# Performance work log

Measured on AMD Instinct MI355X. Metric: run time of the kernel, lower is better.

Reference implementation:

```python
import jax, jax.numpy as jnp
import numpy as np

DRUG_NUM, DIS_NUM, HIDE_DIM = 60000, 40000, 128
HOPS, N_LAYERS, N_HEADS, FFN_DIM, N_EDGES = 7, 2, 4, 512, 800000
N_NODES = DRUG_NUM + DIS_NUM


def _ln(x, s, b, eps=1e-5):
    m = jnp.mean(x, axis=-1, keepdims=True)
    v = jnp.var(x, axis=-1, keepdims=True)
    return (x - m) * jax.lax.rsqrt(v + eps) * s + b


def setup_inputs() -> dict:
    ks = jax.random.split(jax.random.key(0), 16)
    L, D, F = N_LAYERS, HIDE_DIM, FFN_DIM
    sd = 0.05  # param init scale
    n = lambda k, shape, s=sd: jax.random.normal(k, shape, jnp.float32) * s
    kk = jax.random.split(ks[15], 12)
    return {
        'ifTraining': 0,
        'uid': jax.random.randint(ks[0], (256,), 0, DRUG_NUM, jnp.int64 if jax.config.jax_enable_x64 else jnp.int32),
        'iid': jax.random.randint(ks[1], (256,), 0, DIS_NUM, jnp.int64 if jax.config.jax_enable_x64 else jnp.int32),
        'norm': 1,
        'drug_emb': n(ks[2], (DRUG_NUM, D), 0.1),
        'dis_emb': n(ks[3], (DIS_NUM, D), 0.1),
        'edge_src': jax.random.randint(ks[4], (N_EDGES,), 0, N_NODES, jnp.int32),
        'edge_dst': jax.random.randint(ks[5], (N_EDGES,), 0, N_NODES, jnp.int32),
        'edge_val': jax.random.uniform(ks[6], (N_EDGES,), jnp.float32) * 0.1,  # normalized adj values
        'att_w': n(ks[7], (D, D)), 'att_b': jnp.zeros((D,), jnp.float32),
        'ln1_s': jnp.ones((L, D), jnp.float32), 'ln1_b': jnp.zeros((L, D), jnp.float32),
        'q_w': n(kk[0], (L, D, D)), 'q_b': jnp.zeros((L, D), jnp.float32),
        'k_w': n(kk[1], (L, D, D)), 'k_b': jnp.zeros((L, D), jnp.float32),
        'v_w': n(kk[2], (L, D, D)), 'v_b': jnp.zeros((L, D), jnp.float32),
        'o_w': n(kk[3], (L, D, D)), 'o_b': jnp.zeros((L, D), jnp.float32),
        'ln2_s': jnp.ones((L, D), jnp.float32), 'ln2_b': jnp.zeros((L, D), jnp.float32),
        'f1_w': n(kk[4], (L, D, F)), 'f1_b': jnp.zeros((L, F), jnp.float32),
        'f2_w': n(kk[5], (L, F, D)), 'f2_b': jnp.zeros((L, D), jnp.float32),
        'fln_s': jnp.ones((D,), jnp.float32), 'fln_b': jnp.zeros((D,), jnp.float32),
        'attn_w': n(kk[6], (2 * D, 1)), 'attn_b': jnp.zeros((1,), jnp.float32),
    }


def reference(ifTraining, uid, iid, norm, drug_emb, dis_emb, edge_src, edge_dst, edge_val,
              att_w, att_b, ln1_s, ln1_b, q_w, q_b, k_w, k_b, v_w, v_b, o_w, o_b,
              ln2_s, ln2_b, f1_w, f1_b, f2_w, f2_b, fln_s, fln_b, attn_w, attn_b):
    N, D, S, dh = N_NODES, HIDE_DIM, HOPS + 1, HIDE_DIM // N_HEADS
    # ---- re_features: K sparse-adjacency hops over concatenated embeddings ----
    x = jnp.concatenate([drug_emb, dis_emb], axis=0)  # [N, D]
    feats = [x]
    for _ in range(HOPS):
        msgs = x[edge_src] * edge_val[:, None]          # [E, D] gather
        x = jax.ops.segment_sum(msgs, edge_dst, num_segments=N)  # [N, D] scatter-add
        feats.append(x)
    nf = jnp.stack(feats, axis=1)                        # [N, S, D]
    # ---- graph-transformer over the hop sequence (eval: dropout = identity) ----
    h = nf @ att_w + att_b                               # [N, S, D]
    for l in range(N_LAYERS):
        y = _ln(h, ln1_s[l], ln1_b[l])
        q = (y @ q_w[l] + q_b[l]).reshape(N, S, N_HEADS, dh)
        k = (y @ k_w[l] + k_b[l]).reshape(N, S, N_HEADS, dh)
        v = (y @ v_w[l] + v_b[l]).reshape(N, S, N_HEADS, dh)
        a = jnp.einsum('nshd,nthd->nhst', q, k) * (dh ** -0.5)
        a = jax.nn.softmax(a, axis=-1)                   # [N, H, S, S]
        y = jnp.einsum('nhst,nthd->nshd', a, v).reshape(N, S, D)
        h = h + (y @ o_w[l] + o_b[l])
        y = _ln(h, ln2_s[l], ln2_b[l])
        h = h + (jax.nn.gelu(y @ f1_w[l] + f1_b[l]) @ f2_w[l] + f2_b[l])
    out = _ln(h, fln_s, fln_b)
    # ---- readout: node token + softmax attention over hop tokens ----
    node = out[:, 0, :]                                  # [N, D]
    neigh = out[:, 1:, :]                                # [N, HOPS, D]
    target = jnp.broadcast_to(node[:, None, :], neigh.shape)
    att = jnp.concatenate([target, neigh], axis=-1) @ attn_w + attn_b  # [N, HOPS, 1]
    att = jax.nn.softmax(att, axis=1)
    final = node + jnp.sum(neigh * att, axis=1)          # [N, D]
    return final[:DRUG_NUM], final[DRUG_NUM:]
```

## Files before the change

kernel.cpp:

```cpp
#include <hip/hip_runtime.h>
#include <hip/hip_bf16.h>

typedef __hip_bfloat16 bf16;
typedef __attribute__((ext_vector_type(8))) short s16x8;
typedef __attribute__((ext_vector_type(4))) float f32x4;

#define NDRUG 60000
#define NDIS  40000
#define NN    100000
#define DIM   128
#define NHOPS 7
#define NEDGE 800000
#define NSB   98

__device__ __forceinline__ float u2f(unsigned short u) {
    union { unsigned int i; float f; } c; c.i = ((unsigned int)u) << 16; return c.f;
}
__device__ __forceinline__ ushort f2u(float f) {
    bf16 h = __float2bfloat16(f);
    return *reinterpret_cast<ushort*>(&h);
}


__global__ void k_init(const float* __restrict__ drug, const float* __restrict__ dis,
                       ushort* __restrict__ nf) {
    int i = blockIdx.x * 256 + threadIdx.x;
    if (i >= NN * 32) return;
    int n = i >> 5, g = (i & 31) << 2;
    const float* sp = (n < NDRUG) ? drug + (size_t)n * 128 + g
                                  : dis + (size_t)(n - NDRUG) * 128 + g;
    float4 v = *(const float4*)sp;
    ushort4 o;
    o.x = f2u(v.x); o.y = f2u(v.y); o.z = f2u(v.z); o.w = f2u(v.w);
    *(ushort4*)(nf + (size_t)n * 1024 + g) = o;
}

__global__ void k_count(const int* __restrict__ edst, int* __restrict__ cnt) {
    int e = blockIdx.x * 256 + threadIdx.x;
    if (e < NEDGE) atomicAdd(&cnt[edst[e]], 1);
}

__global__ void k_scanA(const int* __restrict__ cnt, int* __restrict__ incl,
                        int* __restrict__ btot) {
    __shared__ int part[1024];
    int b = blockIdx.x, t = threadIdx.x;
    int i = b * 1024 + t;
    part[t] = (i < NN) ? cnt[i] : 0;
    __syncthreads();
    for (int o = 1; o < 1024; o <<= 1) {
        int u = (t >= o) ? part[t - o] : 0;
        __syncthreads();
        part[t] += u;
        __syncthreads();
    }
    if (i < NN) incl[i] = part[t];
    if (t == 1023) btot[b] = part[1023];
}

__global__ void k_scanB(const int* __restrict__ btot, int* __restrict__ boff) {
    if (threadIdx.x == 0) {
        int run = 0;
        for (int b = 0; b < NSB; b++) { boff[b] = run; run += btot[b]; }
        boff[NSB] = run;
    }
}

__global__ void k_scanC(const int* __restrict__ cnt, const int* __restrict__ incl,
                        const int* __restrict__ boff, int* __restrict__ rp) {
    int i = blockIdx.x * 256 + threadIdx.x;
    if (i < NN) rp[i] = incl[i] - cnt[i] + boff[i >> 10];
    if (i == 0) rp[NN] = boff[NSB];
}

__global__ void k_copyrp(const int* __restrict__ rp, int* __restrict__ cur) {
    int i = blockIdx.x * 256 + threadIdx.x;
    if (i < NN) cur[i] = rp[i];
}

__global__ void k_scatter(const int* __restrict__ esrc, const int* __restrict__ edst,
                          const float* __restrict__ eval, int* __restrict__ cur,
                          int* __restrict__ ssrc, float* __restrict__ sval) {
    int e = blockIdx.x * 256 + threadIdx.x;
    if (e >= NEDGE) return;
    int d = edst[e];
    int pos = atomicAdd(&cur[d], 1);
    ssrc[pos] = esrc[e];
    sval[pos] = eval[e];
}

__global__ void k_hopg(ushort* __restrict__ nf, const int* __restrict__ rp,
                       const int* __restrict__ ssrc, const float* __restrict__ sval, int s) {
    int t = blockIdx.x * 256 + threadIdx.x;
    if (t >= NN * 32) return;
    int n = t >> 5, d0 = (t & 31) << 2;
    int e0 = rp[n], e1 = rp[n + 1];
    float4 a = make_float4(0.f, 0.f, 0.f, 0.f);
    for (int e = e0; e < e1; e++) {
        int src = ssrc[e];
        float val = sval[e];
        ushort4 u = *(const ushort4*)(nf + (size_t)src * 1024 + (size_t)(s - 1) * 128 + d0);
        a.x += u2f(u.x) * val; a.y += u2f(u.y) * val;
        a.z += u2f(u.z) * val; a.w += u2f(u.w) * val;
    }
    ushort4 o;
    o.x = f2u(a.x); o.y = f2u(a.y); o.z = f2u(a.z); o.w = f2u(a.w);
    *(ushort4*)(nf + (size_t)n * 1024 + (size_t)s * 128 + d0) = o;
}


__global__ void k_pack(const float* __restrict__ W, ushort* __restrict__ P, int K, int Nout) {
    int idx = blockIdx.x * 256 + threadIdx.x;
    int tot = (Nout >> 4) * (K >> 3) * 16;
    if (idx >= tot) return;
    int c = idx & 15;
    int r = idx >> 4;
    int kb = r % (K >> 3);
    int nt = r / (K >> 3);
    ushort o[8];
    #pragma unroll
    for (int i = 0; i < 8; i++)
        o[i] = f2u(W[(size_t)(kb * 8 + i) * Nout + nt * 16 + c]);
    uint4 v;
    v.x = (uint)o[0] | ((uint)o[1] << 16);
    v.y = (uint)o[2] | ((uint)o[3] << 16);
    v.z = (uint)o[4] | ((uint)o[5] << 16);
    v.w = (uint)o[6] | ((uint)o[7] << 16);
    *(uint4*)(P + (size_t)idx * 8) = v;
}

__global__ void k_catb(const float* __restrict__ qb, const float* __restrict__ kb,
                       const float* __restrict__ vb, float* __restrict__ o) {
    int i = threadIdx.x;
    o[i] = (i < 128) ? qb[i] : ((i < 256) ? kb[i - 128] : vb[i - 256]);
}


template <int ACT, int ADD, int OUTBF, int NTPW>
__global__ void k_mgemm(const ushort* __restrict__ X, const ushort* __restrict__ Wp,
                        const float* __restrict__ bias, void* __restrict__ Yv,
                        int M, int K, int Nout) {
    int w = threadIdx.x >> 6, lane = threadIdx.x & 63;
    int lr = lane & 15, lg = lane >> 4;
    int m0 = blockIdx.x * 16;
    int kb8 = K >> 3;
    int row = m0 + lr; if (row > M - 1) row = M - 1;
    const ushort* ap = X + (size_t)row * K + lg * 8;
    f32x4 acc[NTPW] = {};
    for (int k0 = 0; k0 < K; k0 += 32, ap += 32) {
        s16x8 af = *(const s16x8*)ap;
        int kb = (k0 >> 3) + lg;
        #pragma unroll
        for (int t = 0; t < NTPW; t++) {
            int nt = w + t * 4;
            const ushort* bp = Wp + (((size_t)nt * kb8 + kb) * 16 + lr) * 8;
            s16x8 bf_ = *(const s16x8*)bp;
            acc[t] = __builtin_amdgcn_mfma_f32_16x16x32_bf16(af, bf_, acc[t], 0, 0, 0);
        }
    }
    #pragma unroll
    for (int t = 0; t < NTPW; t++) {
        int n = (w + t * 4) * 16 + lr;
        float bv = bias[n];
        #pragma unroll
        for (int j = 0; j < 4; j++) {
            int m = m0 + lg * 4 + j;
            if (m >= M) continue;
            float v = acc[t][j] + bv;
            if (ACT == 1) {
                float x = v;
                float z = 0.7978845608028654f * (x + 0.044715f * x * x * x);
                v = x / (1.0f + __expf(-2.0f * z));
            }
            if (OUTBF) {
                ((ushort*)Yv)[(size_t)m * Nout + n] = f2u(v);
            } else if (ADD) {
                ((float*)Yv)[(size_t)m * Nout + n] += v;
            } else {
                ((float*)Yv)[(size_t)m * Nout + n] = v;
            }
        }
    }
}


__global__ void k_layer(float* __restrict__ H,
                        const ushort* __restrict__ Wqkv, const ushort* __restrict__ Wo,
                        const ushort* __restrict__ Wf1, const ushort* __restrict__ Wf2,
                        const float* __restrict__ s1v, const float* __restrict__ b1v,
                        const float* __restrict__ bqkv, const float* __restrict__ bo,
                        const float* __restrict__ s2v, const float* __restrict__ b2v,
                        const float* __restrict__ bf1, const float* __restrict__ bf2,
                        int M) {
    __shared__ float  h[16][132];
    __shared__ ushort ylds[16][136];
    __shared__ ushort big[16][520];
    __shared__ float  as_[2][256];
    int tid = threadIdx.x;
    int w = tid >> 6, lane = tid & 63;
    int lr = lane & 15, lg = lane >> 4;
    int m0 = blockIdx.x * 16;

    #pragma unroll
    for (int i = 0; i < 2; i++) {
        int gi = i * 256 + tid;
        int row = gi >> 5, c4 = (gi & 31) << 2;
        int grow = m0 + row; if (grow > M - 1) grow = M - 1;
        *(float4*)&h[row][c4] = *(const float4*)(H + (size_t)grow * 128 + c4);
    }
    __syncthreads();

    #pragma unroll
    for (int i = 0; i < 4; i++) {
        int row = w * 4 + i;
        float2 x = *(const float2*)&h[row][lane * 2];
        float sum = x.x + x.y, sq = x.x * x.x + x.y * x.y;
        #pragma unroll
        for (int o = 32; o; o >>= 1) { sum += __shfl_xor(sum, o); sq += __shfl_xor(sq, o); }
        float mean = sum * (1.f / 128.f);
        float inv = rsqrtf(sq * (1.f / 128.f) - mean * mean + 1e-5f);
        float y0 = (x.x - mean) * inv * s1v[lane * 2 + 0] + b1v[lane * 2 + 0];
        float y1 = (x.y - mean) * inv * s1v[lane * 2 + 1] + b1v[lane * 2 + 1];
        *(uint*)&ylds[row][lane * 2] = (uint)f2u(y0) | ((uint)f2u(y1) << 16);
    }
    __syncthreads();

    {
        f32x4 acc[6] = {};
        for (int k0 = 0; k0 < 128; k0 += 32) {
            s16x8 af = *(const s16x8*)&ylds[lr][lg * 8 + k0];
            int kb = (k0 >> 3) + lg;
            #pragma unroll
            for (int t = 0; t < 6; t++) {
                int nt = w + t * 4;
                const ushort* bp = Wqkv + (((size_t)nt * 16 + kb) * 16 + lr) * 8;
                s16x8 bf_ = *(const s16x8*)bp;
                acc[t] = __builtin_amdgcn_mfma_f32_16x16x32_bf16(af, bf_, acc[t], 0, 0, 0);
            }
        }
        #pragma unroll
        for (int t = 0; t < 6; t++) {
            int n = (w + t * 4) * 16 + lr;
            float bv = bqkv[n];
            #pragma unroll
            for (int j = 0; j < 4; j++) big[lg * 4 + j][n] = f2u(acc[t][j] + bv);
        }
    }
    __syncthreads();

    if (w < 2) {
        int hh = lane >> 4, s_ = (lane >> 1) & 7, p = lane & 1;
        const float scale = 0.17677669529663687f;
        float dots[4];
        float mx = -1e30f;
        #pragma unroll
        for (int t4 = 0; t4 < 4; t4++) {
            int t = p * 4 + t4;
            float dot = 0.f;
            #pragma unroll
            for (int d = 0; d < 32; d++)
                dot += u2f(big[w * 8 + s_][hh * 32 + d]) * u2f(big[w * 8 + t][128 + hh * 32 + d]);
            dots[t4] = dot * scale;
            mx = fmaxf(mx, dots[t4]);
        }
        mx = fmaxf(mx, __shfl_xor(mx, 1));
        float sum = 0.f, e4[4];
        #pragma unroll
        for (int t4 = 0; t4 < 4; t4++) { e4[t4] = __expf(dots[t4] - mx); sum += e4[t4]; }
        sum += __shfl_xor(sum, 1);
        float rinv = 1.f / sum;
        #pragma unroll
        for (int t4 = 0; t4 < 4; t4++) as_[w][hh * 64 + s_ * 8 + p * 4 + t4] = e4[t4] * rinv;
    }
    __syncthreads();

    {
        int nd = w & 1, hf = w >> 1;
        #pragma unroll
        for (int i = 0; i < 8; i++) {
            int o = hf * 512 + i * 64 + lane;
            int ss = o >> 7, rem = o & 127, h2 = rem >> 5, dd = rem & 31;
            float accv = 0.f;
            #pragma unroll
            for (int t = 0; t < 8; t++)
                accv += as_[nd][h2 * 64 + ss * 8 + t] * u2f(big[nd * 8 + t][256 + h2 * 32 + dd]);
            ylds[nd * 8 + ss][rem] = f2u(accv);
        }
    }
    __syncthreads();

    {
        f32x4 acc[2] = {};
        for (int k0 = 0; k0 < 128; k0 += 32) {
            s16x8 af = *(const s16x8*)&ylds[lr][lg * 8 + k0];
            int kb = (k0 >> 3) + lg;
            #pragma unroll
            for (int t = 0; t < 2; t++) {
                int nt = w + t * 4;
                const ushort* bp = Wo + (((size_t)nt * 16 + kb) * 16 + lr) * 8;
                s16x8 bf_ = *(const s16x8*)bp;
                acc[t] = __builtin_amdgcn_mfma_f32_16x16x32_bf16(af, bf_, acc[t], 0, 0, 0);
            }
        }
        #pragma unroll
        for (int t = 0; t < 2; t++) {
            int n = (w + t * 4) * 16 + lr;
            float bv = bo[n];
            #pragma unroll
            for (int j = 0; j < 4; j++) h[lg * 4 + j][n] += acc[t][j] + bv;
        }
    }
    __syncthreads();

    #pragma unroll
    for (int i = 0; i < 4; i++) {
        int row = w * 4 + i;
        float2 x = *(const float2*)&h[row][lane * 2];
        float sum = x.x + x.y, sq = x.x * x.x + x.y * x.y;
        #pragma unroll
        for (int o = 32; o; o >>= 1) { sum += __shfl_xor(sum, o); sq += __shfl_xor(sq, o); }
        float mean = sum * (1.f / 128.f);
        float inv = rsqrtf(sq * (1.f / 128.f) - mean * mean + 1e-5f);
        float y0 = (x.x - mean) * inv * s2v[lane * 2 + 0] + b2v[lane * 2 + 0];
        float y1 = (x.y - mean) * inv * s2v[lane * 2 + 1] + b2v[lane * 2 + 1];
        *(uint*)&ylds[row][lane * 2] = (uint)f2u(y0) | ((uint)f2u(y1) << 16);
    }
    __syncthreads();

    {
        f32x4 acc[8] = {};
        for (int k0 = 0; k0 < 128; k0 += 32) {
            s16x8 af = *(const s16x8*)&ylds[lr][lg * 8 + k0];
            int kb = (k0 >> 3) + lg;
            #pragma unroll
            for (int t = 0; t < 8; t++) {
                int nt = w + t * 4;
                const ushort* bp = Wf1 + (((size_t)nt * 16 + kb) * 16 + lr) * 8;
                s16x8 bf_ = *(const s16x8*)bp;
                acc[t] = __builtin_amdgcn_mfma_f32_16x16x32_bf16(af, bf_, acc[t], 0, 0, 0);
            }
        }
        #pragma unroll
        for (int t = 0; t < 8; t++) {
            int n = (w + t * 4) * 16 + lr;
            float bv = bf1[n];
            #pragma unroll
            for (int j = 0; j < 4; j++) {
                float x = acc[t][j] + bv;
                float z = 0.7978845608028654f * (x + 0.044715f * x * x * x);
                big[lg * 4 + j][n] = f2u(x / (1.0f + __expf(-2.0f * z)));
            }
        }
    }
    __syncthreads();

    {
        f32x4 acc[2] = {};
        for (int k0 = 0; k0 < 512; k0 += 32) {
            s16x8 af = *(const s16x8*)&big[lr][lg * 8 + k0];
            int kb = (k0 >> 3) + lg;
            #pragma unroll
            for (int t = 0; t < 2; t++) {
                int nt = w + t * 4;
                const ushort* bp = Wf2 + (((size_t)nt * 64 + kb) * 16 + lr) * 8;
                s16x8 bf_ = *(const s16x8*)bp;
                acc[t] = __builtin_amdgcn_mfma_f32_16x16x32_bf16(af, bf_, acc[t], 0, 0, 0);
            }
        }
        #pragma unroll
        for (int t = 0; t < 2; t++) {
            int n = (w + t * 4) * 16 + lr;
            float bv = bf2[n];
            #pragma unroll
            for (int j = 0; j < 4; j++) h[lg * 4 + j][n] += acc[t][j] + bv;
        }
    }
    __syncthreads();

    #pragma unroll
    for (int i = 0; i < 2; i++) {
        int gi = i * 256 + tid;
        int row = gi >> 5, c4 = (gi & 31) << 2;
        int grow = m0 + row;
        if (grow < M) *(float4*)(H + (size_t)grow * 128 + c4) = *(const float4*)&h[row][c4];
    }
}


__global__ void k_pool(const float* __restrict__ Hc, const float* __restrict__ fs,
                       const float* __restrict__ fb, const float* __restrict__ aw,
                       const float* __restrict__ ab, float* __restrict__ out,
                       int Nc, int n0g) {
    int w = threadIdx.x >> 6, lane = threadIdx.x & 63;
    int nl = blockIdx.x * 4 + w;
    if (nl >= Nc) return;
    const float* hp = Hc + (size_t)nl * 1024;
    float s0 = fs[lane * 2], s1 = fs[lane * 2 + 1];
    float b0 = fb[lane * 2], b1 = fb[lane * 2 + 1];
    float2 yl[8];
    #pragma unroll
    for (int s = 0; s < 8; s++) {
        float2 x = *(const float2*)(hp + s * DIM + lane * 2);
        float sum = x.x + x.y, sq = x.x * x.x + x.y * x.y;
        #pragma unroll
        for (int o = 32; o; o >>= 1) { sum += __shfl_xor(sum, o); sq += __shfl_xor(sq, o); }
        float mean = sum * (1.f / 128.f);
        float inv = rsqrtf(sq * (1.f / 128.f) - mean * mean + 1e-5f);
        yl[s].x = (x.x - mean) * inv * s0 + b0;
        yl[s].y = (x.y - mean) * inv * s1 + b1;
    }
    float awn0 = aw[lane * 2], awn1 = aw[lane * 2 + 1];
    float awh0 = aw[128 + lane * 2], awh1 = aw[128 + lane * 2 + 1];
    float abv = ab[0];
    float lg[7];
    #pragma unroll
    for (int s = 0; s < 7; s++) {
        float part = yl[0].x * awn0 + yl[0].y * awn1 + yl[s + 1].x * awh0 + yl[s + 1].y * awh1;
        #pragma unroll
        for (int o = 32; o; o >>= 1) part += __shfl_xor(part, o);
        lg[s] = part + abv;
    }
    float mx = lg[0];
    #pragma unroll
    for (int s = 1; s < 7; s++) mx = fmaxf(mx, lg[s]);
    float sum = 0.f;
    #pragma unroll
    for (int s = 0; s < 7; s++) { lg[s] = __expf(lg[s] - mx); sum += lg[s]; }
    float rinv = 1.f / sum;
    float2 f = yl[0];
    #pragma unroll
    for (int s = 0; s < 7; s++) { f.x += lg[s] * rinv * yl[s + 1].x; f.y += lg[s] * rinv * yl[s + 1].y; }
    size_t ob = (size_t)(n0g + nl) * DIM + lane * 2;
    out[ob + 0] = f.x;
    out[ob + 1] = f.y;
}


extern "C" void kernel_launch(void* const* d_in, const int* in_sizes, int n_in,
                              void* d_out, int out_size, void* d_ws, size_t ws_size,
                              hipStream_t stream) {
    const float* drug  = (const float*)d_in[4];
    const float* dis   = (const float*)d_in[5];
    const int*   esrc  = (const int*)d_in[6];
    const int*   edst  = (const int*)d_in[7];
    const float* eval  = (const float*)d_in[8];
    const float* att_w = (const float*)d_in[9];
    const float* att_b = (const float*)d_in[10];
    const float* ln1_s = (const float*)d_in[11];
    const float* ln1_b = (const float*)d_in[12];
    const float* q_w   = (const float*)d_in[13];
    const float* q_b   = (const float*)d_in[14];
    const float* k_w   = (const float*)d_in[15];
    const float* k_b   = (const float*)d_in[16];
    const float* v_w   = (const float*)d_in[17];
    const float* v_b   = (const float*)d_in[18];
    const float* o_w   = (const float*)d_in[19];
    const float* o_b   = (const float*)d_in[20];
    const float* ln2_s = (const float*)d_in[21];
    const float* ln2_b = (const float*)d_in[22];
    const float* f1_w  = (const float*)d_in[23];
    const float* f1_b  = (const float*)d_in[24];
    const float* f2_w  = (const float*)d_in[25];
    const float* f2_b  = (const float*)d_in[26];
    const float* fln_s = (const float*)d_in[27];
    const float* fln_b = (const float*)d_in[28];
    const float* aw    = (const float*)d_in[29];
    const float* ab    = (const float*)d_in[30];
    float* out = (float*)d_out;

    char* ws = (char*)d_ws;
    size_t nfB = (size_t)NN * 1024 * 2;
    ushort* nf = (ushort*)ws;
    size_t off = (nfB + 255) & ~(size_t)255;

    ushort* wpk = (ushort*)(ws + off);
    size_t offCsr = off + (1 << 20);
    int*   rp   = (int*)(ws + offCsr);
    int*   cnt  = rp + (NN + 1);
    int*   ssrc = cnt + NN;
    float* sval = (float*)(ssrc + NEDGE);
    int*   incl = (int*)(sval + NEDGE);
    int*   btot = incl + NN;
    int*   boff = btot + 128;
    size_t csrInts = (size_t)(NN + 1) + NN + NEDGE + NEDGE + NN + 256;
    size_t off2 = offCsr + ((csrInts * 4 + 255) & ~(size_t)255);

    size_t scratchB = (ws_size > off2) ? ws_size - off2 : 0;
    long long ncMax = (long long)(scratchB / 4096);
    ncMax &= ~1LL;
    if (ncMax < 2) ncMax = 2;
    int Nc = (int)((ncMax < NN) ? ncMax : NN);
    int nchunks = (NN + Nc - 1) / Nc;
    Nc = (NN + nchunks - 1) / nchunks;
    if (Nc & 1) Nc++;
    float* hbuf = (float*)(ws + off2);

    size_t wpAtt = 0;
    size_t wpQKV[2], wpO[2], wpF1[2], wpF2[2];
    {
        size_t p = 16384;
        for (int l = 0; l < 2; l++) {
            wpQKV[l] = p; p += 49152;
            wpO[l]   = p; p += 16384;
            wpF1[l]  = p; p += 65536;
            wpF2[l]  = p; p += 65536;
        }
    }
    float* qkvB = (float*)(wpk + 409600);

    {
        int b128 = (16384 / 8 + 255) / 256;
        int b512 = (65536 / 8 + 255) / 256;
        k_pack<<<b128, 256, 0, stream>>>(att_w, wpk + wpAtt, 128, 128);
        for (int l = 0; l < 2; l++) {
            k_pack<<<b128, 256, 0, stream>>>(q_w + (size_t)l * 16384, wpk + wpQKV[l], 128, 128);
            k_pack<<<b128, 256, 0, stream>>>(k_w + (size_t)l * 16384, wpk + wpQKV[l] + 16384, 128, 128);
            k_pack<<<b128, 256, 0, stream>>>(v_w + (size_t)l * 16384, wpk + wpQKV[l] + 32768, 128, 128);
            k_pack<<<b128, 256, 0, stream>>>(o_w + (size_t)l * 16384, wpk + wpO[l], 128, 128);
            k_pack<<<b512, 256, 0, stream>>>(f1_w + (size_t)l * 65536, wpk + wpF1[l], 128, 512);
            k_pack<<<b512, 256, 0, stream>>>(f2_w + (size_t)l * 65536, wpk + wpF2[l], 512, 128);
            k_catb<<<1, 384, 0, stream>>>(q_b + l * 128, k_b + l * 128, v_b + l * 128, qkvB + l * 384);
        }
    }

    (void)hipMemsetAsync(cnt, 0, (size_t)NN * 4, stream);
    k_count<<<(NEDGE + 255) / 256, 256, 0, stream>>>(edst, cnt);
    k_scanA<<<NSB, 1024, 0, stream>>>(cnt, incl, btot);
    k_scanB<<<1, 64, 0, stream>>>(btot, boff);
    k_scanC<<<(NN + 255) / 256, 256, 0, stream>>>(cnt, incl, boff, rp);
    k_copyrp<<<(NN + 255) / 256, 256, 0, stream>>>(rp, cnt);
    k_scatter<<<(NEDGE + 255) / 256, 256, 0, stream>>>(esrc, edst, eval, cnt, ssrc, sval);

    k_init<<<(NN * 32 + 255) / 256, 256, 0, stream>>>(drug, dis, nf);
    for (int s = 1; s <= NHOPS; s++)
        k_hopg<<<(NN * 32 + 255) / 256, 256, 0, stream>>>(nf, rp, ssrc, sval, s);

    for (int c = 0; c < nchunks; c++) {
        int cn0 = c * Nc;
        int cn = NN - cn0; if (cn > Nc) cn = Nc;
        if (cn <= 0) break;
        int Mc = cn * 8;
        int mb = (Mc + 15) / 16;
        int nb = (cn + 3) / 4;

        k_mgemm<0, 0, 0, 2><<<mb, 256, 0, stream>>>(nf + (size_t)cn0 * 1024, wpk + wpAtt,
                                                    att_b, hbuf, Mc, 128, 128);
        for (int l = 0; l < 2; l++) {
            k_layer<<<mb, 256, 0, stream>>>(hbuf, wpk + wpQKV[l], wpk + wpO[l],
                                            wpk + wpF1[l], wpk + wpF2[l],
                                            ln1_s + l * 128, ln1_b + l * 128,
                                            qkvB + l * 384, o_b + l * 128,
                                            ln2_s + l * 128, ln2_b + l * 128,
                                            f1_b + l * 512, f2_b + l * 128, Mc);
        }
        k_pool<<<nb, 256, 0, stream>>>(hbuf, fln_s, fln_b, aw, ab, out, cn, cn0);
    }
    (void)in_sizes; (void)n_in; (void)out_size;
}
```

Measured before the change: 2.918 ms.

## Compute per-head attention scores and PV product with MFMA in layer kernel

```diff
diff --git a/kernel.cpp b/kernel.cpp
--- a/kernel.cpp
+++ b/kernel.cpp
@@ -194,7 +194,7 @@
     __shared__ float  h[16][132];
     __shared__ ushort ylds[16][136];
     __shared__ ushort big[16][520];
-    __shared__ float  as_[2][256];
+    __shared__ ushort psm[4][16][16];
     int tid = threadIdx.x;
     int w = tid >> 6, lane = tid & 63;
     int lr = lane & 15, lg = lane >> 4;
@@ -247,43 +247,46 @@
     }
     __syncthreads();
 
-    if (w < 2) {
-        int hh = lane >> 4, s_ = (lane >> 1) & 7, p = lane & 1;
+    {
+        f32x4 zero = {0.f, 0.f, 0.f, 0.f};
+        s16x8 aq = *(const s16x8*)&big[lr][w * 32 + lg * 8];
+        s16x8 bk = *(const s16x8*)&big[lr][128 + w * 32 + lg * 8];
+        f32x4 c = __builtin_amdgcn_mfma_f32_16x16x32_bf16(aq, bk, zero, 0, 0, 0);
         const float scale = 0.17677669529663687f;
-        float dots[4];
-        float mx = -1e30f;
-        #pragma unroll
-        for (int t4 = 0; t4 < 4; t4++) {
-            int t = p * 4 + t4;
-            float dot = 0.f;
-            #pragma unroll
-            for (int d = 0; d < 32; d++)
-                dot += u2f(big[w * 8 + s_][hh * 32 + d]) * u2f(big[w * 8 + t][128 + hh * 32 + d]);
-            dots[t4] = dot * scale;
-            mx = fmaxf(mx, dots[t4]);
-        }
-        mx = fmaxf(mx, __shfl_xor(mx, 1));
-        float sum = 0.f, e4[4];
-        #pragma unroll
-        for (int t4 = 0; t4 < 4; t4++) { e4[t4] = __expf(dots[t4] - mx); sum += e4[t4]; }
-        sum += __shfl_xor(sum, 1);
-        float rinv = 1.f / sum;
-        #pragma unroll
-        for (int t4 = 0; t4 < 4; t4++) as_[w][hh * 64 + s_ * 8 + p * 4 + t4] = e4[t4] * rinv;
-    }
-    __syncthreads();
-
-    {
-        int nd = w & 1, hf = w >> 1;
-        #pragma unroll
-        for (int i = 0; i < 8; i++) {
-            int o = hf * 512 + i * 64 + lane;
-            int ss = o >> 7, rem = o & 127, h2 = rem >> 5, dd = rem & 31;
-            float accv = 0.f;
-            #pragma unroll
-            for (int t = 0; t < 8; t++)
-                accv += as_[nd][h2 * 64 + ss * 8 + t] * u2f(big[nd * 8 + t][256 + h2 * 32 + dd]);
-            ylds[nd * 8 + ss][rem] = f2u(accv);
+        #pragma unroll
+        for (int j = 0; j < 4; j++) {
+            float v = c[j] * scale;
+            float mx = v;
+            mx = fmaxf(mx, __shfl_xor(mx, 1));
+            mx = fmaxf(mx, __shfl_xor(mx, 2));
+            mx = fmaxf(mx, __shfl_xor(mx, 4));
+            float e = __expf(v - mx);
+            float sum = e;
+            sum += __shfl_xor(sum, 1);
+            sum += __shfl_xor(sum, 2);
+            sum += __shfl_xor(sum, 4);
+            int row = lg * 4 + j;
+            bool valid = ((lr >> 3) == (row >> 3));
+            psm[w][row][lr] = valid ? f2u(e / sum) : (ushort)0;
+        }
+    }
+
+    {
+        f32x4 zero = {0.f, 0.f, 0.f, 0.f};
+        #pragma unroll
+        for (int nh = 0; nh < 2; nh++) {
+            s16x8 aP = {};
+            s16x8 bV = {};
+            if (lg < 2) {
+                aP = *(const s16x8*)&psm[w][lr][lg * 8];
+                #pragma unroll
+                for (int i = 0; i < 8; i++)
+                    bV[i] = (short)big[lg * 8 + i][256 + w * 32 + nh * 16 + lr];
+            }
+            f32x4 o = __builtin_amdgcn_mfma_f32_16x16x32_bf16(aP, bV, zero, 0, 0, 0);
+            #pragma unroll
+            for (int j = 0; j < 4; j++)
+                ylds[lg * 4 + j][w * 32 + nh * 16 + lr] = f2u(o[j]);
         }
     }
     __syncthreads();
```

After: 2.813 ms, median of 2. -3.6%, faster.
